# Optimization experiments

Measured on AMD Instinct MI355X. Metric: run time of the kernel, lower is better.

Reference implementation:

```python
import jax, jax.numpy as jnp
import numpy as np

B, S, H, DH, RD = 4, 512, 8, 64, 64
DM = H * DH  # hidden_size = 512


def setup_inputs() -> dict:
    key = jax.random.key(0)
    ks = jax.random.split(key, 8)
    x = jax.random.normal(ks[0], (B, S, DM), dtype=jnp.float32)
    graph_matrix = jax.random.randint(ks[1], (B, S, S), 0, 2).astype(jnp.int32)
    rel_embeddings = jax.random.normal(ks[2], (B, S, S, RD), dtype=jnp.float32)
    scale = 0.02
    Wq = jax.random.normal(ks[3], (DM, DM), dtype=jnp.float32) * scale
    Wk = jax.random.normal(ks[4], (DM, DM), dtype=jnp.float32) * scale
    Wv = jax.random.normal(ks[5], (DM, DM), dtype=jnp.float32) * scale
    Wr = jax.random.normal(ks[6], (DH, RD), dtype=jnp.float32) * scale
    br = jnp.zeros((DH,), dtype=jnp.float32)
    return {"input_tensor": x, "graph_matrix": graph_matrix,
            "rel_embeddings": rel_embeddings, "Wq": Wq, "Wk": Wk,
            "Wv": Wv, "Wr": Wr, "br": br}


def reference(input_tensor, graph_matrix, rel_embeddings, Wq, Wk, Wv, Wr, br):
    b, s, dm = input_tensor.shape
    h, dh = H, dm // H

    def heads(t):  # (b,s,dm) -> (b,h,s,dh)
        return t.reshape(b, s, h, dh).transpose(0, 2, 1, 3)

    q = heads(input_tensor @ Wq.T)
    k = heads(input_tensor @ Wk.T)
    v = heads(input_tensor @ Wv.T)

    # rel_to_hidden: (b,s,s,rel_dim) -> (b,s,s,dh); shared across heads
    rel_h = rel_embeddings @ Wr.T + br

    # matmul_rel(q, k, rel) == q.k^T + sum_d q[...,q_pos,d] * rel[...,q_pos,k_pos,d]
    # computed WITHOUT materializing the (b,h,s,s,dh) intermediate
    scores = (jnp.einsum('bhqd,bhkd->bhqk', q, k)
              + jnp.einsum('bhqd,bqkd->bhqk', q, rel_h))
    scores = scores / (dh ** 0.5)

    # adjacency masking: (1 - graph) * -1e9, broadcast over heads
    neg_inf_mask = (1.0 - graph_matrix.astype(scores.dtype)) * -1e9
    scores = scores + neg_inf_mask[:, None, :, :]

    probs = jax.nn.softmax(scores, axis=-1)  # dropout = identity at inference
    ctx = jnp.einsum('bhqk,bhkd->bqhd', probs, v).reshape(b, s, dm)
    return ctx
```

## Files before the change

### kernel.cpp

```cpp
#include <hip/hip_runtime.h>


typedef __attribute__((ext_vector_type(4))) float f32x4;
typedef __attribute__((ext_vector_type(8))) short s16x8;
typedef __attribute__((ext_vector_type(4))) unsigned short u16x4;
typedef __attribute__((ext_vector_type(8))) unsigned short u16x8;

typedef const __attribute__((address_space(1))) unsigned int* gas_ptr;
typedef __attribute__((address_space(3))) unsigned int* las_ptr;

__device__ __forceinline__ void gload16(const void* g, void* l) {
  __builtin_amdgcn_global_load_lds((gas_ptr)g, (las_ptr)l, 16, 0, 0);
}

__device__ __forceinline__ unsigned short f2bf(float f) {
  union { float f; unsigned int u; } x; x.f = f;
  return (unsigned short)((x.u + 0x7fffu + ((x.u >> 16) & 1u)) >> 16);
}
__device__ __forceinline__ float bf2f(unsigned short u) {
  union { unsigned int u; float f; } x; x.u = ((unsigned int)u) << 16;
  return x.f;
}

__global__ __launch_bounds__(256) void prep(
    const float* __restrict__ x, const float* __restrict__ Wq,
    const float* __restrict__ Wk, const float* __restrict__ Wv,
    const float* __restrict__ Wr, unsigned short* __restrict__ xb,
    unsigned short* __restrict__ Wb) {
  int blk = blockIdx.x, t = threadIdx.x;
  if (blk < 1024) {
    int i = (blk * 256 + t) * 4;
    f32x4 v = *(const f32x4*)(x + i);
    u16x4 u; u.x = f2bf(v.x); u.y = f2bf(v.y); u.z = f2bf(v.z); u.w = f2bf(v.w);
    *(u16x4*)(xb + i) = u;
  } else if (blk < 1792) {
    int i = ((blk - 1024) * 256 + t) * 4;
    const float* src = (i < 262144) ? Wq : (i < 524288 ? Wk : Wv);
    f32x4 v = *(const f32x4*)(src + (i & 262143));
    u16x4 u; u.x = f2bf(v.x); u.y = f2bf(v.y); u.z = f2bf(v.z); u.w = f2bf(v.w);
    *(u16x4*)(Wb + i) = u;
  } else {
    int o = (blk - 1792) * 256 + t;
    int c = o & 511, n = o >> 9, h = n >> 6, r = n & 63;
    float acc = 0.f;
#pragma unroll 8
    for (int d = 0; d < 64; ++d) acc += Wr[d * 64 + r] * Wq[(h * 64 + d) * 512 + c];
    Wb[3 * 262144 + o] = f2bf(acc);
  }
}

#define G64_STAGE(MAT, SRC, LD, M0, K0)                                       \
  _Pragma("unroll") for (int is = 0; is < 2; ++is) {                          \
    int fc = is * 256 + w * 64 + lane;                                        \
    int row = fc >> 3, cl = fc & 7;                                           \
    gload16(SRC + (long)(M0 + row) * LD + K0 + ((cl ^ (row & 7)) * 8),        \
            (char*)MAT + (size_t)fc * 16);                                    \
  }
#define G128_STAGE(MAT, SRC, LD, M0, K0)                                      \
  _Pragma("unroll") for (int is = 0; is < 4; ++is) {                          \
    int fc = (is * 4 + w) * 64 + lane;                                        \
    int row = fc >> 3, cl = fc & 7;                                           \
    gload16(SRC + (long)(M0 + row) * LD + K0 + ((cl ^ (row & 7)) * 8),        \
            (char*)MAT + (size_t)fc * 16);                                    \
  }

#define G128_FRAGS(AF, BF)                                                    \
  _Pragma("unroll") for (int kk = 0; kk < 2; ++kk) {                          \
    _Pragma("unroll") for (int i = 0; i < 4; ++i) {                           \
      int ra = wm + 16 * i + fr;                                              \
      AF[kk][i] = *(const s16x8*)((const char*)As +                           \
                  ((size_t)ra * 8 + ((kk * 4 + g) ^ (ra & 7))) * 16);         \
      int rb = wn + 16 * i + fr;                                              \
      BF[kk][i] = *(const s16x8*)((const char*)Bs +                           \
                  ((size_t)rb * 8 + ((kk * 4 + g) ^ (rb & 7))) * 16);         \
    }                                                                         \
  }

__global__ __launch_bounds__(256) void gemm_qkv_g(
    const unsigned short* __restrict__ xb, const unsigned short* __restrict__ Wb,
    unsigned short* __restrict__ Qb, unsigned short* __restrict__ Kb,
    unsigned short* __restrict__ Vt, unsigned short* __restrict__ QRb) {
  int z = blockIdx.z;
  const unsigned short* Bm = Wb + (long)z * 262144;
  int m0 = blockIdx.x * 64, n0 = blockIdx.y * 64;
  __shared__ alignas(16) unsigned short As[64 * 64];
  __shared__ alignas(16) unsigned short Bs[64 * 64];
  int t = threadIdx.x, lane = t & 63, w = t >> 6;
  int wm = (w >> 1) * 32, wn = (w & 1) * 32;
  int fr = lane & 15, g = lane >> 4;
  f32x4 acc[2][2] = {};
  for (int k0 = 0; k0 < 512; k0 += 64) {
    __syncthreads();
    G64_STAGE(As, xb, 512, m0, k0)
    G64_STAGE(Bs, Bm, 512, n0, k0)
    __syncthreads();
#pragma unroll
    for (int kh = 0; kh < 2; ++kh) {
      s16x8 a0, a1, b0, b1;
      {
        int ra = wm + fr;
        a0 = *(const s16x8*)((const char*)As + ((size_t)ra * 8 + ((kh * 4 + g) ^ (ra & 7))) * 16);
        int ra1 = wm + 16 + fr;
        a1 = *(const s16x8*)((const char*)As + ((size_t)ra1 * 8 + ((kh * 4 + g) ^ (ra1 & 7))) * 16);
        int rb = wn + fr;
        b0 = *(const s16x8*)((const char*)Bs + ((size_t)rb * 8 + ((kh * 4 + g) ^ (rb & 7))) * 16);
        int rb1 = wn + 16 + fr;
        b1 = *(const s16x8*)((const char*)Bs + ((size_t)rb1 * 8 + ((kh * 4 + g) ^ (rb1 & 7))) * 16);
      }
      acc[0][0] = __builtin_amdgcn_mfma_f32_16x16x32_bf16(a0, b0, acc[0][0], 0, 0, 0);
      acc[0][1] = __builtin_amdgcn_mfma_f32_16x16x32_bf16(a0, b1, acc[0][1], 0, 0, 0);
      acc[1][0] = __builtin_amdgcn_mfma_f32_16x16x32_bf16(a1, b0, acc[1][0], 0, 0, 0);
      acc[1][1] = __builtin_amdgcn_mfma_f32_16x16x32_bf16(a1, b1, acc[1][1], 0, 0, 0);
    }
  }
  int rbase = g * 4;
#pragma unroll
  for (int i = 0; i < 2; ++i)
#pragma unroll
    for (int j = 0; j < 2; ++j)
#pragma unroll
      for (int jj = 0; jj < 4; ++jj) {
        int row = m0 + wm + 16 * i + rbase + jj;
        int cc  = n0 + wn + 16 * j + fr;
        int b = row >> 9, s = row & 511, h = cc >> 6, d = cc & 63;
        unsigned short val = f2bf(acc[i][j][jj]);
        if (z == 0)      Qb[(((long)(b * 8 + h)) * 512 + s) * 64 + d] = val;
        else if (z == 1) Kb[(((long)(b * 8 + h)) * 512 + s) * 64 + d] = val;
        else if (z == 2) Vt[(((long)(b * 8 + h)) * 64 + d) * 512 + s] = val;
        else             QRb[(long)row * 512 + cc] = val;
      }
}

__global__ __launch_bounds__(256) void gemm128_c16(
    const unsigned short* __restrict__ Ag, const unsigned short* __restrict__ Bg,
    unsigned short* __restrict__ Cb) {
  int z = blockIdx.z;
  const unsigned short* A = Ag + (long)z * 32768;
  const unsigned short* Bm = Bg + (long)z * 32768;
  long coff = (long)z * 262144;
  int m0 = blockIdx.x * 128, n0 = blockIdx.y * 128;
  __shared__ alignas(16) unsigned short As[128 * 64];
  __shared__ alignas(16) unsigned short Bs[128 * 64];
  int t = threadIdx.x, lane = t & 63, w = t >> 6;
  int wm = (w >> 1) * 64, wn = (w & 1) * 64;
  int fr = lane & 15, g = lane >> 4;
  f32x4 acc[4][4] = {};
  G128_STAGE(As, A, 64, m0, 0)
  G128_STAGE(Bs, Bm, 64, n0, 0)
  __syncthreads();
  s16x8 af[2][4], bf_[2][4];
  G128_FRAGS(af, bf_)
#pragma unroll
  for (int kk = 0; kk < 2; ++kk)
#pragma unroll
    for (int i = 0; i < 4; ++i)
#pragma unroll
      for (int j = 0; j < 4; ++j)
        acc[i][j] = __builtin_amdgcn_mfma_f32_16x16x32_bf16(af[kk][i], bf_[kk][j],
                                                            acc[i][j], 0, 0, 0);
  int rbase = g * 4;
#pragma unroll
  for (int i = 0; i < 4; ++i)
#pragma unroll
    for (int j = 0; j < 4; ++j)
#pragma unroll
      for (int jj = 0; jj < 4; ++jj) {
        long row = m0 + wm + 16 * i + rbase + jj;
        int cc   = n0 + wn + 16 * j + fr;
        Cb[coff + row * 512 + cc] = f2bf(acc[i][j][jj]);
      }
}

__global__ __launch_bounds__(256) void gemm_nt(
    const unsigned short* __restrict__ A, int lda, long sA,
    const unsigned short* __restrict__ Bm, int ldb, long sB,
    float* __restrict__ Cv, int ldc, int subC, long sC1, long sC2, int K) {
  int z = blockIdx.z;
  A  += (long)z * sA;
  Bm += (long)z * sB;
  long coff = (long)(z / subC) * sC1 + (long)(z % subC) * sC2;
  int m0 = blockIdx.x * 64, n0 = blockIdx.y * 64;
  __shared__ alignas(16) unsigned short As[64][40];
  __shared__ alignas(16) unsigned short Bs[64][40];
  int t = threadIdx.x, lane = t & 63, w = t >> 6;
  int wm = (w >> 1) * 32, wn = (w & 1) * 32;
  int fr = lane & 15, fk = (lane >> 4) * 8;
  int sr = t >> 2, sc = (t & 3) * 8;
  f32x4 acc[2][2] = {};
  for (int k0 = 0; k0 < K; k0 += 32) {
    __syncthreads();
    *(u16x8*)&As[sr][sc] = *(const u16x8*)(A + (long)(m0 + sr) * lda + k0 + sc);
    *(u16x8*)&Bs[sr][sc] = *(const u16x8*)(Bm + (long)(n0 + sr) * ldb + k0 + sc);
    __syncthreads();
    s16x8 a0 = *(const s16x8*)&As[wm + fr][fk];
    s16x8 a1 = *(const s16x8*)&As[wm + 16 + fr][fk];
    s16x8 b0 = *(const s16x8*)&Bs[wn + fr][fk];
    s16x8 b1 = *(const s16x8*)&Bs[wn + 16 + fr][fk];
    acc[0][0] = __builtin_amdgcn_mfma_f32_16x16x32_bf16(a0, b0, acc[0][0], 0, 0, 0);
    acc[0][1] = __builtin_amdgcn_mfma_f32_16x16x32_bf16(a0, b1, acc[0][1], 0, 0, 0);
    acc[1][0] = __builtin_amdgcn_mfma_f32_16x16x32_bf16(a1, b0, acc[1][0], 0, 0, 0);
    acc[1][1] = __builtin_amdgcn_mfma_f32_16x16x32_bf16(a1, b1, acc[1][1], 0, 0, 0);
  }
  int rbase = (lane >> 4) * 4;
#pragma unroll
  for (int i = 0; i < 2; ++i)
#pragma unroll
    for (int j = 0; j < 2; ++j)
#pragma unroll
      for (int jj = 0; jj < 4; ++jj) {
        long row = m0 + wm + 16 * i + rbase + jj;
        int cc   = n0 + wn + 16 * j + fr;
        Cv[coff + row * ldc + cc] = acc[i][j][jj];
      }
}

__global__ __launch_bounds__(256) void rel_fused(
    const float* __restrict__ rel, const int* __restrict__ graph,
    const unsigned short* __restrict__ Sqkb, const unsigned short* __restrict__ QRb,
    unsigned short* __restrict__ P) {
  int b = blockIdx.x >> 9, q = blockIdx.x & 511;
  __shared__ float s_lds[8][512];
  __shared__ unsigned short qr16[16][64];
  __shared__ int idxL[512];
  __shared__ int cntL[8];
  int t = threadIdx.x, lane = t & 63, w = t >> 6;

#pragma unroll
  for (int i = 0; i < 4; ++i) {
    f32x4 mv = {-8e9f, -8e9f, -8e9f, -8e9f};
    *(f32x4*)&s_lds[0][t * 4 + i * 1024] = mv;
  }
  if (t < 64) {
    u16x8 v = *(const u16x8*)(QRb + ((long)(b * 512 + q)) * 512 + t * 8);
    *(u16x8*)&qr16[t >> 3][(t & 7) * 8] = v;
  } else if (t < 128) {
    u16x8 zv = {};
    *(u16x8*)&qr16[8 + ((t - 64) >> 3)][((t - 64) & 7) * 8] = zv;
  }
  const int* grow = graph + ((long)(b * 512 + q)) * 512;
  int gA = grow[t], gB = grow[t + 256];
  unsigned long long mA = __ballot(gA != 0);
  unsigned long long mB = __ballot(gB != 0);
  unsigned long long below = (lane == 63) ? ~0ull : ((1ull << (lane + 1)) - 1);
  below >>= 1;
  int pA = __popcll(mA & below), pB = __popcll(mB & below);
  if (lane == 0) { cntL[w] = __popcll(mA); cntL[4 + w] = __popcll(mB); }
  __syncthreads();
  int base[8];
  int nact = 0;
#pragma unroll
  for (int g2 = 0; g2 < 8; ++g2) { base[g2] = nact; nact += cntL[g2]; }
  if (gA) idxL[base[w] + pA] = t;
  if (gB) idxL[base[4 + w] + pB] = t + 256;
  __syncthreads();

  int fr = lane & 15, fk = (lane >> 4) * 8;
  s16x8 aq0 = *(const s16x8*)&qr16[fr][fk];
  s16x8 aq1 = *(const s16x8*)&qr16[fr][32 + fk];
  const float* rg = rel + ((long)(b * 512 + q)) * 32768;
  int nchunk = (nact + 63) >> 6;

  for (int c = 0; c < nchunk; ++c) {
    int slot = c * 64 + 16 * w + fr;
    int krow = (slot < nact) ? idxL[slot] : 0;
    const float* rp = rg + krow * 64;
    f32x4 r0 = *(const f32x4*)(rp + fk);
    f32x4 r1 = *(const f32x4*)(rp + fk + 4);
    f32x4 r2 = *(const f32x4*)(rp + 32 + fk);
    f32x4 r3 = *(const f32x4*)(rp + 32 + fk + 4);
    s16x8 b0, b1;
    b0[0] = (short)f2bf(r0.x); b0[1] = (short)f2bf(r0.y);
    b0[2] = (short)f2bf(r0.z); b0[3] = (short)f2bf(r0.w);
    b0[4] = (short)f2bf(r1.x); b0[5] = (short)f2bf(r1.y);
    b0[6] = (short)f2bf(r1.z); b0[7] = (short)f2bf(r1.w);
    b1[0] = (short)f2bf(r2.x); b1[1] = (short)f2bf(r2.y);
    b1[2] = (short)f2bf(r2.z); b1[3] = (short)f2bf(r2.w);
    b1[4] = (short)f2bf(r3.x); b1[5] = (short)f2bf(r3.y);
    b1[6] = (short)f2bf(r3.z); b1[7] = (short)f2bf(r3.w);
    f32x4 acc = {};
    acc = __builtin_amdgcn_mfma_f32_16x16x32_bf16(aq0, b0, acc, 0, 0, 0);
    acc = __builtin_amdgcn_mfma_f32_16x16x32_bf16(aq1, b1, acc, 0, 0, 0);
    if (lane < 32 && slot < nact) {
      int hb = (lane >> 4) * 4;
#pragma unroll
      for (int j = 0; j < 4; ++j) s_lds[hb + j][krow] = acc[j];
    }
  }
  __syncthreads();

  for (int h = w; h < 8; h += 4) {
    const unsigned short* srow = Sqkb + (((long)(b * 8 + h)) * 512 + q) * 512;
    float vals[8];
    float m = -3.0e38f;
#pragma unroll
    for (int i = 0; i < 8; ++i) {
      int k = lane + 64 * i;
      vals[i] = (s_lds[h][k] + bf2f(srow[k])) * 0.125f;
      m = fmaxf(m, vals[i]);
    }
#pragma unroll
    for (int off = 32; off >= 1; off >>= 1) m = fmaxf(m, __shfl_xor(m, off));
    float sum = 0.f;
#pragma unroll
    for (int i = 0; i < 8; ++i) { vals[i] = __expf(vals[i] - m); sum += vals[i]; }
#pragma unroll
    for (int off = 32; off >= 1; off >>= 1) sum += __shfl_xor(sum, off);
    float inv = 1.0f / sum;
    unsigned short* Pg = P + (((long)(b * 8 + h)) * 512 + q) * 512;
#pragma unroll
    for (int i = 0; i < 8; ++i) Pg[lane + 64 * i] = f2bf(vals[i] * inv);
  }
}

extern "C" void kernel_launch(void* const* d_in, const int* in_sizes, int n_in,
                              void* d_out, int out_size, void* d_ws, size_t ws_size,
                              hipStream_t stream) {
  const float* x     = (const float*)d_in[0];
  const int*   graph = (const int*)d_in[1];
  const float* rel   = (const float*)d_in[2];
  const float* Wq    = (const float*)d_in[3];
  const float* Wk    = (const float*)d_in[4];
  const float* Wv    = (const float*)d_in[5];
  const float* Wr    = (const float*)d_in[6];
  float* out = (float*)d_out;

  char* wp = (char*)d_ws;
  unsigned short* xb  = (unsigned short*)wp; wp += (size_t)2 * 1048576;
  unsigned short* Wb  = (unsigned short*)wp; wp += (size_t)2 * 4 * 262144;
  unsigned short* Qb  = (unsigned short*)wp; wp += (size_t)2 * 1048576;
  unsigned short* Kb  = (unsigned short*)wp; wp += (size_t)2 * 1048576;
  unsigned short* Vt  = (unsigned short*)wp; wp += (size_t)2 * 1048576;
  unsigned short* QRb = (unsigned short*)wp; wp += (size_t)2 * 1048576;
  unsigned short* Sqkb = (unsigned short*)wp; wp += (size_t)2 * 8388608;
  unsigned short* P   = (unsigned short*)wp; wp += (size_t)2 * 8388608;

  prep<<<2816, 256, 0, stream>>>(x, Wq, Wk, Wv, Wr, xb, Wb);

  gemm_qkv_g<<<dim3(32, 8, 4), 256, 0, stream>>>(xb, Wb, Qb, Kb, Vt, QRb);

  gemm128_c16<<<dim3(4, 4, 32), 256, 0, stream>>>(Qb, Kb, Sqkb);

  rel_fused<<<2048, 256, 0, stream>>>(rel, graph, Sqkb, QRb, P);

  gemm_nt<<<dim3(8, 1, 32), 256, 0, stream>>>(
      P, 512, 262144L, Vt, 512, 32768L, out, 512, 8, 262144L, 64L, 512);
}
```

Measured before the change: 74.25 us.

## Prefetch rel rows and score tiles, deepen QKV K-tile, rewrite PV GEMM

```diff
diff --git a/kernel.cpp b/kernel.cpp
--- a/kernel.cpp
+++ b/kernel.cpp
@@ -49,16 +49,16 @@
   }
 }
 
-#define G64_STAGE(MAT, SRC, LD, M0, K0)                                       \
-  _Pragma("unroll") for (int is = 0; is < 2; ++is) {                          \
-    int fc = is * 256 + w * 64 + lane;                                        \
-    int row = fc >> 3, cl = fc & 7;                                           \
+#define G64K128_STAGE(MAT, SRC, LD, M0, K0)                                   \
+  _Pragma("unroll") for (int is = 0; is < 4; ++is) {                          \
+    int fc = is * 256 + t;                                                    \
+    int row = fc >> 4, cl = fc & 15;                                          \
     gload16(SRC + (long)(M0 + row) * LD + K0 + ((cl ^ (row & 7)) * 8),        \
             (char*)MAT + (size_t)fc * 16);                                    \
   }
 #define G128_STAGE(MAT, SRC, LD, M0, K0)                                      \
   _Pragma("unroll") for (int is = 0; is < 4; ++is) {                          \
-    int fc = (is * 4 + w) * 64 + lane;                                        \
+    int fc = is * 256 + t;                                                    \
     int row = fc >> 3, cl = fc & 7;                                           \
     gload16(SRC + (long)(M0 + row) * LD + K0 + ((cl ^ (row & 7)) * 8),        \
             (char*)MAT + (size_t)fc * 16);                                    \
@@ -83,29 +83,29 @@
   int z = blockIdx.z;
   const unsigned short* Bm = Wb + (long)z * 262144;
   int m0 = blockIdx.x * 64, n0 = blockIdx.y * 64;
-  __shared__ alignas(16) unsigned short As[64 * 64];
-  __shared__ alignas(16) unsigned short Bs[64 * 64];
+  __shared__ alignas(16) unsigned short As[64 * 128];
+  __shared__ alignas(16) unsigned short Bs[64 * 128];
   int t = threadIdx.x, lane = t & 63, w = t >> 6;
   int wm = (w >> 1) * 32, wn = (w & 1) * 32;
   int fr = lane & 15, g = lane >> 4;
   f32x4 acc[2][2] = {};
-  for (int k0 = 0; k0 < 512; k0 += 64) {
+  for (int k0 = 0; k0 < 512; k0 += 128) {
     __syncthreads();
-    G64_STAGE(As, xb, 512, m0, k0)
-    G64_STAGE(Bs, Bm, 512, n0, k0)
+    G64K128_STAGE(As, xb, 512, m0, k0)
+    G64K128_STAGE(Bs, Bm, 512, n0, k0)
     __syncthreads();
 #pragma unroll
-    for (int kh = 0; kh < 2; ++kh) {
+    for (int kh = 0; kh < 4; ++kh) {
       s16x8 a0, a1, b0, b1;
       {
         int ra = wm + fr;
-        a0 = *(const s16x8*)((const char*)As + ((size_t)ra * 8 + ((kh * 4 + g) ^ (ra & 7))) * 16);
+        a0 = *(const s16x8*)((const char*)As + ((size_t)ra * 16 + ((kh * 4 + g) ^ (ra & 7))) * 16);
         int ra1 = wm + 16 + fr;
-        a1 = *(const s16x8*)((const char*)As + ((size_t)ra1 * 8 + ((kh * 4 + g) ^ (ra1 & 7))) * 16);
+        a1 = *(const s16x8*)((const char*)As + ((size_t)ra1 * 16 + ((kh * 4 + g) ^ (ra1 & 7))) * 16);
         int rb = wn + fr;
-        b0 = *(const s16x8*)((const char*)Bs + ((size_t)rb * 8 + ((kh * 4 + g) ^ (rb & 7))) * 16);
+        b0 = *(const s16x8*)((const char*)Bs + ((size_t)rb * 16 + ((kh * 4 + g) ^ (rb & 7))) * 16);
         int rb1 = wn + 16 + fr;
-        b1 = *(const s16x8*)((const char*)Bs + ((size_t)rb1 * 8 + ((kh * 4 + g) ^ (rb1 & 7))) * 16);
+        b1 = *(const s16x8*)((const char*)Bs + ((size_t)rb1 * 16 + ((kh * 4 + g) ^ (rb1 & 7))) * 16);
       }
       acc[0][0] = __builtin_amdgcn_mfma_f32_16x16x32_bf16(a0, b0, acc[0][0], 0, 0, 0);
       acc[0][1] = __builtin_amdgcn_mfma_f32_16x16x32_bf16(a0, b1, acc[0][1], 0, 0, 0);
@@ -171,47 +171,54 @@
       }
 }
 
-__global__ __launch_bounds__(256) void gemm_nt(
-    const unsigned short* __restrict__ A, int lda, long sA,
-    const unsigned short* __restrict__ Bm, int ldb, long sB,
-    float* __restrict__ Cv, int ldc, int subC, long sC1, long sC2, int K) {
+__global__ __launch_bounds__(256) void gemm_pv(
+    const unsigned short* __restrict__ Pg, const unsigned short* __restrict__ Vtg,
+    float* __restrict__ out) {
   int z = blockIdx.z;
-  A  += (long)z * sA;
-  Bm += (long)z * sB;
-  long coff = (long)(z / subC) * sC1 + (long)(z % subC) * sC2;
-  int m0 = blockIdx.x * 64, n0 = blockIdx.y * 64;
-  __shared__ alignas(16) unsigned short As[64][40];
-  __shared__ alignas(16) unsigned short Bs[64][40];
+  const unsigned short* A = Pg + (long)z * 262144;
+  const unsigned short* Bm = Vtg + (long)z * 32768;
+  long coff = (long)(z >> 3) * 262144 + (long)(z & 7) * 64;
+  int m0 = blockIdx.x * 32;
+  __shared__ alignas(16) unsigned short As[32 * 64];
+  __shared__ alignas(16) unsigned short Bs[64 * 64];
   int t = threadIdx.x, lane = t & 63, w = t >> 6;
-  int wm = (w >> 1) * 32, wn = (w & 1) * 32;
-  int fr = lane & 15, fk = (lane >> 4) * 8;
-  int sr = t >> 2, sc = (t & 3) * 8;
-  f32x4 acc[2][2] = {};
-  for (int k0 = 0; k0 < K; k0 += 32) {
+  int wm = (w >> 1) * 16, wn = (w & 1) * 32;
+  int fr = lane & 15, g = lane >> 4;
+  f32x4 acc[2] = {};
+  for (int k0 = 0; k0 < 512; k0 += 64) {
     __syncthreads();
-    *(u16x8*)&As[sr][sc] = *(const u16x8*)(A + (long)(m0 + sr) * lda + k0 + sc);
-    *(u16x8*)&Bs[sr][sc] = *(const u16x8*)(Bm + (long)(n0 + sr) * ldb + k0 + sc);
+    {
+      int fc = t, row = fc >> 3, cl = fc & 7;
+      gload16(A + (long)(m0 + row) * 512 + k0 + ((cl ^ (row & 7)) * 8),
+              (char*)As + (size_t)fc * 16);
+    }
+#pragma unroll
+    for (int is = 0; is < 2; ++is) {
+      int fc = is * 256 + t, row = fc >> 3, cl = fc & 7;
+      gload16(Bm + (long)row * 512 + k0 + ((cl ^ (row & 7)) * 8),
+              (char*)Bs + (size_t)fc * 16);
+    }
     __syncthreads();
-    s16x8 a0 = *(const s16x8*)&As[wm + fr][fk];
-    s16x8 a1 = *(const s16x8*)&As[wm + 16 + fr][fk];
-    s16x8 b0 = *(const s16x8*)&Bs[wn + fr][fk];
-    s16x8 b1 = *(const s16x8*)&Bs[wn + 16 + fr][fk];
-    acc[0][0] = __builtin_amdgcn_mfma_f32_16x16x32_bf16(a0, b0, acc[0][0], 0, 0, 0);
-    acc[0][1] = __builtin_amdgcn_mfma_f32_16x16x32_bf16(a0, b1, acc[0][1], 0, 0, 0);
-    acc[1][0] = __builtin_amdgcn_mfma_f32_16x16x32_bf16(a1, b0, acc[1][0], 0, 0, 0);
-    acc[1][1] = __builtin_amdgcn_mfma_f32_16x16x32_bf16(a1, b1, acc[1][1], 0, 0, 0);
-  }
-  int rbase = (lane >> 4) * 4;
-#pragma unroll
-  for (int i = 0; i < 2; ++i)
-#pragma unroll
-    for (int j = 0; j < 2; ++j)
-#pragma unroll
-      for (int jj = 0; jj < 4; ++jj) {
-        long row = m0 + wm + 16 * i + rbase + jj;
-        int cc   = n0 + wn + 16 * j + fr;
-        Cv[coff + row * ldc + cc] = acc[i][j][jj];
-      }
+#pragma unroll
+    for (int kh = 0; kh < 2; ++kh) {
+      int ra = wm + fr;
+      s16x8 a0 = *(const s16x8*)((const char*)As + ((size_t)ra * 8 + ((kh * 4 + g) ^ (ra & 7))) * 16);
+      int rb0 = wn + fr, rb1 = wn + 16 + fr;
+      s16x8 b0 = *(const s16x8*)((const char*)Bs + ((size_t)rb0 * 8 + ((kh * 4 + g) ^ (rb0 & 7))) * 16);
+      s16x8 b1 = *(const s16x8*)((const char*)Bs + ((size_t)rb1 * 8 + ((kh * 4 + g) ^ (rb1 & 7))) * 16);
+      acc[0] = __builtin_amdgcn_mfma_f32_16x16x32_bf16(a0, b0, acc[0], 0, 0, 0);
+      acc[1] = __builtin_amdgcn_mfma_f32_16x16x32_bf16(a0, b1, acc[1], 0, 0, 0);
+    }
+  }
+  int rbase = g * 4;
+#pragma unroll
+  for (int j = 0; j < 2; ++j)
+#pragma unroll
+    for (int jj = 0; jj < 4; ++jj) {
+      long row = m0 + wm + rbase + jj;
+      int cc = wn + 16 * j + fr;
+      out[coff + row * 512 + cc] = acc[j][jj];
+    }
 }
 
 __global__ __launch_bounds__(256) void rel_fused(
@@ -221,7 +228,7 @@
   int b = blockIdx.x >> 9, q = blockIdx.x & 511;
   __shared__ float s_lds[8][512];
   __shared__ unsigned short qr16[16][64];
-  __shared__ int idxL[512];
+  __shared__ unsigned short idxL[512];
   __shared__ int cntL[8];
   int t = threadIdx.x, lane = t & 63, w = t >> 6;
 
@@ -236,6 +243,14 @@
   } else if (t < 128) {
     u16x8 zv = {};
     *(u16x8*)&qr16[8 + ((t - 64) >> 3)][((t - 64) & 7) * 8] = zv;
+  }
+  unsigned short sq[2][8];
+#pragma unroll
+  for (int hh = 0; hh < 2; ++hh) {
+    int h = w + hh * 4;
+    const unsigned short* srow = Sqkb + (((long)(b * 8 + h)) * 512 + q) * 512;
+#pragma unroll
+    for (int i = 0; i < 8; ++i) sq[hh][i] = srow[lane + 64 * i];
   }
   const int* grow = graph + ((long)(b * 512 + q)) * 512;
   int gA = grow[t], gB = grow[t + 256];
@@ -250,8 +265,8 @@
   int nact = 0;
 #pragma unroll
   for (int g2 = 0; g2 < 8; ++g2) { base[g2] = nact; nact += cntL[g2]; }
-  if (gA) idxL[base[w] + pA] = t;
-  if (gB) idxL[base[4 + w] + pB] = t + 256;
+  if (gA) idxL[base[w] + pA] = (unsigned short)t;
+  if (gB) idxL[base[4 + w] + pB] = (unsigned short)(t + 256);
   __syncthreads();
 
   int fr = lane & 15, fk = (lane >> 4) * 8;
@@ -260,42 +275,51 @@
   const float* rg = rel + ((long)(b * 512 + q)) * 32768;
   int nchunk = (nact + 63) >> 6;
 
+  int slot_c = 16 * w + fr;
+  int krow_c = (slot_c < nact) ? (int)idxL[slot_c] : 0;
+  const float* rp0 = rg + krow_c * 64;
+  f32x4 c0 = *(const f32x4*)(rp0 + fk);
+  f32x4 c1 = *(const f32x4*)(rp0 + fk + 4);
+  f32x4 c2 = *(const f32x4*)(rp0 + 32 + fk);
+  f32x4 c3 = *(const f32x4*)(rp0 + 32 + fk + 4);
   for (int c = 0; c < nchunk; ++c) {
-    int slot = c * 64 + 16 * w + fr;
-    int krow = (slot < nact) ? idxL[slot] : 0;
-    const float* rp = rg + krow * 64;
-    f32x4 r0 = *(const f32x4*)(rp + fk);
-    f32x4 r1 = *(const f32x4*)(rp + fk + 4);
-    f32x4 r2 = *(const f32x4*)(rp + 32 + fk);
-    f32x4 r3 = *(const f32x4*)(rp + 32 + fk + 4);
+    int slot_n = (c + 1) * 64 + 16 * w + fr;
+    int krow_n = (slot_n < nact) ? (int)idxL[slot_n] : 0;
+    const float* rpn = rg + krow_n * 64;
+    f32x4 n0 = *(const f32x4*)(rpn + fk);
+    f32x4 n1 = *(const f32x4*)(rpn + fk + 4);
+    f32x4 n2 = *(const f32x4*)(rpn + 32 + fk);
+    f32x4 n3 = *(const f32x4*)(rpn + 32 + fk + 4);
     s16x8 b0, b1;
-    b0[0] = (short)f2bf(r0.x); b0[1] = (short)f2bf(r0.y);
-    b0[2] = (short)f2bf(r0.z); b0[3] = (short)f2bf(r0.w);
-    b0[4] = (short)f2bf(r1.x); b0[5] = (short)f2bf(r1.y);
-    b0[6] = (short)f2bf(r1.z); b0[7] = (short)f2bf(r1.w);
-    b1[0] = (short)f2bf(r2.x); b1[1] = (short)f2bf(r2.y);
-    b1[2] = (short)f2bf(r2.z); b1[3] = (short)f2bf(r2.w);
-    b1[4] = (short)f2bf(r3.x); b1[5] = (short)f2bf(r3.y);
-    b1[6] = (short)f2bf(r3.z); b1[7] = (short)f2bf(r3.w);
+    b0[0] = (short)f2bf(c0.x); b0[1] = (short)f2bf(c0.y);
+    b0[2] = (short)f2bf(c0.z); b0[3] = (short)f2bf(c0.w);
+    b0[4] = (short)f2bf(c1.x); b0[5] = (short)f2bf(c1.y);
+    b0[6] = (short)f2bf(c1.z); b0[7] = (short)f2bf(c1.w);
+    b1[0] = (short)f2bf(c2.x); b1[1] = (short)f2bf(c2.y);
+    b1[2] = (short)f2bf(c2.z); b1[3] = (short)f2bf(c2.w);
+    b1[4] = (short)f2bf(c3.x); b1[5] = (short)f2bf(c3.y);
+    b1[6] = (short)f2bf(c3.z); b1[7] = (short)f2bf(c3.w);
     f32x4 acc = {};
     acc = __builtin_amdgcn_mfma_f32_16x16x32_bf16(aq0, b0, acc, 0, 0, 0);
     acc = __builtin_amdgcn_mfma_f32_16x16x32_bf16(aq1, b1, acc, 0, 0, 0);
-    if (lane < 32 && slot < nact) {
+    if (lane < 32 && slot_c < nact) {
       int hb = (lane >> 4) * 4;
 #pragma unroll
-      for (int j = 0; j < 4; ++j) s_lds[hb + j][krow] = acc[j];
-    }
+      for (int j = 0; j < 4; ++j) s_lds[hb + j][krow_c] = acc[j];
+    }
+    slot_c = slot_n; krow_c = krow_n;
+    c0 = n0; c1 = n1; c2 = n2; c3 = n3;
   }
   __syncthreads();
 
-  for (int h = w; h < 8; h += 4) {
-    const unsigned short* srow = Sqkb + (((long)(b * 8 + h)) * 512 + q) * 512;
+  for (int hh = 0; hh < 2; ++hh) {
+    int h = w + hh * 4;
     float vals[8];
     float m = -3.0e38f;
 #pragma unroll
     for (int i = 0; i < 8; ++i) {
       int k = lane + 64 * i;
-      vals[i] = (s_lds[h][k] + bf2f(srow[k])) * 0.125f;
+      vals[i] = (s_lds[h][k] + bf2f(sq[hh][i])) * 0.125f;
       m = fmaxf(m, vals[i]);
     }
 #pragma unroll
@@ -342,6 +366,5 @@
 
   rel_fused<<<2048, 256, 0, stream>>>(rel, graph, Sqkb, QRb, P);
 
-  gemm_nt<<<dim3(8, 1, 32), 256, 0, stream>>>(
-      P, 512, 262144L, Vt, 512, 32768L, out, 512, 8, 262144L, 64L, 512);
-}
+  gemm_pv<<<dim3(16, 1, 32), 256, 0, stream>>>(P, Vt, out);
+}
```

After: 71.54 us (median of 2 runs). -3.6%, faster.
